# Kernel tuning notes

Hardware: AMD Instinct MI355X
Metric: run time of the kernel (lower is better)

Reference implementation:

```python
import jax, jax.numpy as jnp
import numpy as np

N, E = 50000, 800000
DIN, DH, H, DOUT = 128, 16, 8, 32  # hidden = H*DH = 128
NEG_SLOPE = 0.2


def setup_inputs() -> dict:
    key = jax.random.key(0)
    ks = jax.random.split(key, 10)
    g = lambda k, shape, fan: jax.random.normal(k, shape, jnp.float32) * (1.0 / np.sqrt(fan))
    return {
        "x": jax.random.normal(ks[0], (N, DIN), jnp.float32),
        "edge_index": jax.random.randint(ks[1], (2, E), 0, N, dtype=jnp.int64),
        # layer 1 (GATv2Conv(DIN, DH, heads=H), concat=True)
        "W1_src": g(ks[2], (DIN, H * DH), DIN),
        "W1_dst": g(ks[3], (DIN, H * DH), DIN),
        "b1_src": jnp.zeros((H * DH,), jnp.float32),
        "b1_dst": jnp.zeros((H * DH,), jnp.float32),
        "att1": g(ks[4], (H, DH), DH),
        "bias1": jnp.zeros((H * DH,), jnp.float32),
        # layer 2 (GATv2Conv(H*DH, DOUT, heads=1))
        "W2_src": g(ks[5], (H * DH, DOUT), H * DH),
        "W2_dst": g(ks[6], (H * DH, DOUT), H * DH),
        "b2_src": jnp.zeros((DOUT,), jnp.float32),
        "b2_dst": jnp.zeros((DOUT,), jnp.float32),
        "att2": g(ks[7], (1, DOUT), DOUT),
        "bias2": jnp.zeros((DOUT,), jnp.float32),
    }


def _gatv2(x, src, dst, Wsrc, Wdst, bsrc, bdst, att, bias):
    # GATv2 conv: e_ij = att . LeakyReLU(Wsrc x_j + Wdst x_i); softmax over j->i; out_i = sum alpha_ij * Wsrc x_j
    n = x.shape[0]
    h, c = att.shape
    xs = (x @ Wsrc + bsrc).reshape(n, h, c)  # source transform (messages)
    xd = (x @ Wdst + bdst).reshape(n, h, c)  # target transform
    msg = xs[src]  # [Etot, h, c]
    e = jax.nn.leaky_relu(msg + xd[dst], NEG_SLOPE)
    logits = jnp.einsum('ehc,hc->eh', e, att)  # [Etot, h]
    m = jax.lax.stop_gradient(jax.ops.segment_max(logits, dst, num_segments=n))
    ex = jnp.exp(logits - m[dst])
    denom = jax.ops.segment_sum(ex, dst, num_segments=n)
    alpha = ex / denom[dst]  # edge softmax per target node, per head
    out = jax.ops.segment_sum(alpha[..., None] * msg, dst, num_segments=n)
    return out.reshape(n, h * c) + bias  # concat=True


def reference(x, edge_index, W1_src, W1_dst, b1_src, b1_dst, att1, bias1,
              W2_src, W2_dst, b2_src, b2_dst, att2, bias2):
    n = x.shape[0]
    loop = jnp.arange(n, dtype=edge_index.dtype)  # add_self_loops=True (PyG default)
    src = jnp.concatenate([edge_index[0], loop])
    dst = jnp.concatenate([edge_index[1], loop])
    h1 = _gatv2(x, src, dst, W1_src, W1_dst, b1_src, b1_dst, att1, bias1)
    h1 = jax.nn.elu(h1)
    h2 = _gatv2(h1, src, dst, W2_src, W2_dst, b2_src, b2_dst, att2, bias2)  # heads=1 -> [N, DOUT]
    return jax.nn.log_softmax(h2, axis=1)
```

## Files before the change

kernel.cpp:

```cpp
#include <hip/hip_runtime.h>
#include <math.h>

#define NEG_SLOPE 0.2f

typedef __attribute__((ext_vector_type(8))) _Float16 h8v;
typedef __attribute__((ext_vector_type(2))) _Float16 h2v;
typedef __attribute__((ext_vector_type(4))) float float4v;

__device__ __forceinline__ h2v u2h(unsigned u) { return __builtin_bit_cast(h2v, u); }
__device__ __forceinline__ unsigned h2u(h2v h) { return __builtin_bit_cast(unsigned, h); }
__device__ __forceinline__ unsigned pk16(float a, float b) {
  h2v r; r.x = (_Float16)a; r.y = (_Float16)b;
  return __builtin_bit_cast(unsigned, r);
}
__device__ __forceinline__ unsigned short f16b(float f) {
  return __builtin_bit_cast(unsigned short, (_Float16)f);
}
__device__ __forceinline__ float fdot2(h2v a, h2v b, float c) {
#if __has_builtin(__builtin_amdgcn_fdot2)
  return __builtin_amdgcn_fdot2(a, b, c, false);
#else
  return fmaf((float)a.x, (float)b.x, fmaf((float)a.y, (float)b.y, c));
#endif
}

__device__ __forceinline__ int block_scan256(int v, int tid, int* ws) {
  const int lane = tid & 63, w = tid >> 6;
  int incl = v;
#pragma unroll
  for (int off = 1; off < 64; off <<= 1) {
    int t = __shfl_up(incl, off);
    if (lane >= off) incl += t;
  }
  if (lane == 63) ws[w] = incl;
  __syncthreads();
  if (tid == 0) {
    int s = 0;
#pragma unroll
    for (int i = 0; i < 4; i++) { int t = ws[i]; ws[4 + i] = s; s += t; }
  }
  __syncthreads();
  return incl - v + ws[4 + w];
}

__global__ __launch_bounds__(256) void pack_hist(
    const float* __restrict__ W1s, const float* __restrict__ W1d,
    const float* __restrict__ W2s, const float* __restrict__ W2d,
    unsigned short* __restrict__ B1s, unsigned short* __restrict__ B1d,
    unsigned short* __restrict__ B2s, unsigned short* __restrict__ B2d,
    const int* __restrict__ ei, int* __restrict__ bhist, int N, int E, int NB) {
  int blk = blockIdx.x;
  if (blk < 20) {
    const float* W; unsigned short* Bp; int C, base;
    if (blk < 8)       { W = W1s; Bp = B1s; C = 128; base = blk; }
    else if (blk < 16) { W = W1d; Bp = B1d; C = 128; base = blk - 8; }
    else if (blk < 18) { W = W2s; Bp = B2s; C = 32;  base = blk - 16; }
    else               { W = W2d; Bp = B2d; C = 32;  base = blk - 18; }
    int idx = base * 256 + threadIdx.x;
    int total = (C / 16) * 4 * 64;
    if (idx >= total) return;
    int lane = idx & 63;
    int kc = (idx >> 6) & 3;
    int t = idx >> 8;
    int n = t * 16 + (lane & 15);
    int k0 = kc * 32 + (lane >> 4) * 8;
    unsigned short* o = Bp + (size_t)idx * 8;
#pragma unroll
    for (int j = 0; j < 8; j++) o[j] = f16b(W[(size_t)(k0 + j) * C + n]);
    return;
  }
  blk -= 20;
  __shared__ int cnt[256];
  const int tid = threadIdx.x;
  cnt[tid] = 0;
  __syncthreads();
  const int base = blk * 4096;
  const int vn = min(4096, E - base);
#pragma unroll 4
  for (int j = 0; j < 16; j++) {
    int i = j * 256 + tid;
    if (i < vn) {
      int d = ei[E + base + i];
      d = min(max(d, 0), N - 1);
      atomicAdd(&cnt[d >> 8], 1);
    }
  }
  __syncthreads();
  if (tid < NB && cnt[tid]) atomicAdd(&bhist[tid], cnt[tid]);
}

__global__ __launch_bounds__(256) void bucket_scan(
    const int* __restrict__ bhist, int* __restrict__ bbase,
    int* __restrict__ bcur, int NB) {
  __shared__ int ws[8];
  const int tid = threadIdx.x;
  int v = (tid < NB) ? bhist[tid] : 0;
  int excl = block_scan256(v, tid, ws);
  if (tid <= NB) bbase[tid] = excl;
  if (tid < NB) bcur[tid] = excl;
}

__global__ __launch_bounds__(256) void bucket_sort(
    const int* __restrict__ ei, int* __restrict__ bcur,
    unsigned int* __restrict__ pairs, int N, int E, int NB) {
  __shared__ int cnt[256];
  __shared__ int offs[256];
  __shared__ int gbase[256];
  __shared__ int lcur[256];
  __shared__ int ws[8];
  __shared__ unsigned int packed_s[4096];
  __shared__ unsigned char bucket_of[4096];
  const int tid = threadIdx.x;
  cnt[tid] = 0;
  __syncthreads();
  const int base = blockIdx.x * 4096;
  const int vn = min(4096, E - base);
#pragma unroll 4
  for (int j = 0; j < 16; j++) {
    int i = j * 256 + tid;
    if (i < vn) {
      int d = ei[E + base + i];
      d = min(max(d, 0), N - 1);
      atomicAdd(&cnt[d >> 8], 1);
    }
  }
  __syncthreads();
  int excl = block_scan256(cnt[tid], tid, ws);
  offs[tid] = excl;
  lcur[tid] = excl;
  if (tid < NB && cnt[tid]) gbase[tid] = atomicAdd(&bcur[tid], cnt[tid]);
  __syncthreads();
#pragma unroll 4
  for (int j = 0; j < 16; j++) {
    int i = j * 256 + tid;
    if (i < vn) {
      int s = ei[base + i];
      int d = ei[E + base + i];
      s = min(max(s, 0), N - 1);
      d = min(max(d, 0), N - 1);
      int b = d >> 8;
      int slot = atomicAdd(&lcur[b], 1);
      packed_s[slot] = (unsigned)s | ((unsigned)(d & 255) << 16);
      bucket_of[slot] = (unsigned char)b;
    }
  }
  __syncthreads();
  for (int i = tid; i < vn; i += 256) {
    int b = bucket_of[i];
    pairs[gbase[b] + (i - offs[b])] = packed_s[i];
  }
}

__global__ __launch_bounds__(256) void csr_fine(
    const unsigned int* __restrict__ pairs, const int* __restrict__ bbase,
    int* __restrict__ row_ofs, int* __restrict__ src_sorted, int N, int E, int NB) {
  __shared__ int cnt[256];
  __shared__ int cursor[256];
  __shared__ int ws[8];
  const int tid = threadIdx.x;
  const int b = blockIdx.x;
  const int d0 = b << 8;
  const int nd = min(256, N - d0);
  const int pbase = bbase[b];
  const int pcnt = bbase[b + 1] - pbase;
  const int row_base = pbase + d0;
  cnt[tid] = (tid < nd) ? 1 : 0;
  __syncthreads();
  for (int i = tid; i < pcnt; i += 256) {
    unsigned p = pairs[pbase + i];
    atomicAdd(&cnt[(p >> 16) & 255], 1);
  }
  __syncthreads();
  int excl = block_scan256(cnt[tid], tid, ws);
  if (tid < nd) {
    row_ofs[d0 + tid] = row_base + excl;
    src_sorted[row_base + excl] = d0 + tid;
    cursor[tid] = excl + 1;
  }
  if (b == NB - 1 && tid == 0) row_ofs[N] = E + N;
  __syncthreads();
  for (int i = tid; i < pcnt; i += 256) {
    unsigned p = pairs[pbase + i];
    int dl = (p >> 16) & 255;
    int slot = atomicAdd(&cursor[dl], 1);
    src_sorted[row_base + slot] = (int)(p & 0xffffu);
  }
}

template <int NT, int CVT>
__global__ __launch_bounds__(256) void mfma_xform2(
    const void* __restrict__ Xin,
    const unsigned short* __restrict__ BpS, const unsigned short* __restrict__ BpD,
    const float* __restrict__ bS, const float* __restrict__ bD,
    unsigned int* __restrict__ Ys, unsigned int* __restrict__ Yd, int M) {
  const int wave = threadIdx.x >> 6;
  const int lane = threadIdx.x & 63;
  const int row0 = blockIdx.x * 64 + wave * 16;
  const int m = lane & 15, q = lane >> 4;
  const int arow = min(row0 + m, M - 1);
  h8v a[4];
  if constexpr (CVT) {
    const float* xp = (const float*)Xin + (size_t)arow * 128 + q * 8;
#pragma unroll
    for (int kc = 0; kc < 4; kc++) {
      const float4 f0 = *(const float4*)(xp + kc * 32);
      const float4 f1 = *(const float4*)(xp + kc * 32 + 4);
      uint4 u;
      u.x = pk16(f0.x, f0.y); u.y = pk16(f0.z, f0.w);
      u.z = pk16(f1.x, f1.y); u.w = pk16(f1.z, f1.w);
      a[kc] = __builtin_bit_cast(h8v, u);
    }
  } else {
    const unsigned short* xp = (const unsigned short*)Xin + (size_t)arow * 128 + q * 8;
#pragma unroll
    for (int kc = 0; kc < 4; kc++) a[kc] = *(const h8v*)(xp + kc * 32);
  }
  float4v accS[NT], accD[NT];
#pragma unroll
  for (int t = 0; t < NT; t++) { accS[t] = (float4v)(0.f); accD[t] = (float4v)(0.f); }
#pragma unroll
  for (int kc = 0; kc < 4; kc++) {
#pragma unroll
    for (int t = 0; t < NT; t++) {
      h8v bs = *(const h8v*)(BpS + ((size_t)(t * 4 + kc) * 64 + lane) * 8);
      h8v bd = *(const h8v*)(BpD + ((size_t)(t * 4 + kc) * 64 + lane) * 8);
      accS[t] = __builtin_amdgcn_mfma_f32_16x16x32_f16(a[kc], bs, accS[t], 0, 0, 0);
      accD[t] = __builtin_amdgcn_mfma_f32_16x16x32_f16(a[kc], bd, accD[t], 0, 0, 0);
    }
  }
  const bool even = (m & 1) == 0;
#pragma unroll
  for (int t = 0; t < NT; t++) {
    const int col = t * 16 + m;
    const float bcS = bS[col], bcD = bD[col];
#pragma unroll
    for (int r = 0; r < 4; r++) {
      const int row = row0 + q * 4 + r;
      float vS = accS[t][r] + bcS;
      float vD = accD[t][r] + bcD;
      float pS = __shfl_xor(vS, 1);
      float pD = __shfl_xor(vD, 1);
      if (even && row < M) {
        size_t idx = (size_t)row * (NT * 8) + t * 8 + (m >> 1);
        Ys[idx] = pk16(vS, pS);
        Yd[idx] = pk16(vD, pD);
      }
    }
  }
}

__global__ __launch_bounds__(256) void gat1_fused(
    const int* __restrict__ row_ofs, const int* __restrict__ src_sorted,
    const unsigned int* __restrict__ xsb, const unsigned int* __restrict__ xdb,
    const float* __restrict__ att, const float* __restrict__ bias,
    unsigned int* __restrict__ h1b, int N) {
  const int node = (int)((blockIdx.x * 256u + threadIdx.x) >> 6);
  const int lane = threadIdx.x & 63;
  const int l = lane & 15;
  const int g = lane >> 4;
  if (node >= N) return;
  h2v at2[4], xd[4];
  {
    const float4 a01 = *(const float4*)(att + 8 * l);
    const float4 a23 = *(const float4*)(att + 8 * l + 4);
    at2[0] = u2h(pk16(a01.x, a01.y)); at2[1] = u2h(pk16(a01.z, a01.w));
    at2[2] = u2h(pk16(a23.x, a23.y)); at2[3] = u2h(pk16(a23.z, a23.w));
    const uint4 xdp = *(const uint4*)(xdb + (unsigned)(node * 64 + 4 * l));
    xd[0] = u2h(xdp.x); xd[1] = u2h(xdp.y);
    xd[2] = u2h(xdp.z); xd[3] = u2h(xdp.w);
  }
  h2v ns; ns.x = (_Float16)NEG_SLOPE; ns.y = (_Float16)NEG_SLOPE;
  h2v acc[4];
#pragma unroll
  for (int i = 0; i < 4; i++) acc[i] = (h2v)((_Float16)0.f);
  float den = 0.f;
  const int b = row_ofs[node];
  const int cnt = row_ofs[node + 1] - b;
  for (int base = 0; base < cnt; base += 64) {
    const int rem = cnt - base;
    int sidx = (lane < rem) ? src_sorted[b + base + lane] : node;
    const int nIter = min(16, (rem + 3) >> 2);
    int s = __shfl(sidx, g);
    uint4 mp = *(const uint4*)(xsb + (unsigned)(s * 64 + 4 * l));
    for (int it = 0; it < nIter; it++) {
      const uint4 cur = mp;
      const bool v = (base + 4 * it + g) < cnt;
      if (it + 1 < nIter) {
        int sn = __shfl(sidx, 4 * (it + 1) + g);
        mp = *(const uint4*)(xsb + (unsigned)(sn * 64 + 4 * l));
      }
      const h2v m0 = u2h(cur.x), m1 = u2h(cur.y), m2 = u2h(cur.z), m3 = u2h(cur.w);
      h2v t0 = m0 + xd[0]; h2v r0 = __builtin_elementwise_max(t0, t0 * ns);
      h2v t1 = m1 + xd[1]; h2v r1 = __builtin_elementwise_max(t1, t1 * ns);
      h2v t2 = m2 + xd[2]; h2v r2 = __builtin_elementwise_max(t2, t2 * ns);
      h2v t3 = m3 + xd[3]; h2v r3 = __builtin_elementwise_max(t3, t3 * ns);
      float p = fdot2(r0, at2[0], 0.f);
      p = fdot2(r1, at2[1], p);
      p = fdot2(r2, at2[2], p);
      p = fdot2(r3, at2[3], p);
      p += __shfl_xor(p, 1);
      float ex = v ? __expf(p) : 0.f;
      den += ex;
      h2v exh; exh.x = exh.y = (_Float16)ex;
      acc[0] += m0 * exh;
      acc[1] += m1 * exh;
      acc[2] += m2 * exh;
      acc[3] += m3 * exh;
    }
  }
#pragma unroll
  for (int off = 16; off < 64; off <<= 1) {
#pragma unroll
    for (int i = 0; i < 4; i++) acc[i] += u2h(__shfl_xor(h2u(acc[i]), off));
    den += __shfl_xor(den, off);
  }
  if (lane < 16) {
    const float inv = 1.f / den;
    const float4 bc01 = *(const float4*)(bias + 8 * l);
    const float4 bc23 = *(const float4*)(bias + 8 * l + 4);
    float v0 = fmaf((float)acc[0].x, inv, bc01.x);
    float v1 = fmaf((float)acc[0].y, inv, bc01.y);
    float v2 = fmaf((float)acc[1].x, inv, bc01.z);
    float v3 = fmaf((float)acc[1].y, inv, bc01.w);
    float v4 = fmaf((float)acc[2].x, inv, bc23.x);
    float v5 = fmaf((float)acc[2].y, inv, bc23.y);
    float v6 = fmaf((float)acc[3].x, inv, bc23.z);
    float v7 = fmaf((float)acc[3].y, inv, bc23.w);
    v0 = v0 > 0.f ? v0 : __expf(v0) - 1.f;
    v1 = v1 > 0.f ? v1 : __expf(v1) - 1.f;
    v2 = v2 > 0.f ? v2 : __expf(v2) - 1.f;
    v3 = v3 > 0.f ? v3 : __expf(v3) - 1.f;
    v4 = v4 > 0.f ? v4 : __expf(v4) - 1.f;
    v5 = v5 > 0.f ? v5 : __expf(v5) - 1.f;
    v6 = v6 > 0.f ? v6 : __expf(v6) - 1.f;
    v7 = v7 > 0.f ? v7 : __expf(v7) - 1.f;
    uint4 o;
    o.x = pk16(v0, v1); o.y = pk16(v2, v3);
    o.z = pk16(v4, v5); o.w = pk16(v6, v7);
    *(uint4*)(h1b + (unsigned)(node * 64 + 4 * l)) = o;
  }
}

__global__ __launch_bounds__(256) void gat2_fused(
    const int* __restrict__ row_ofs, const int* __restrict__ src_sorted,
    const unsigned int* __restrict__ xsb, const unsigned int* __restrict__ xdb,
    const float* __restrict__ att, const float* __restrict__ bias,
    float* __restrict__ out, int N) {
  const int node = (int)((blockIdx.x * 256u + threadIdx.x) >> 6);
  const int lane = threadIdx.x & 63;
  const int l = lane & 3;
  const int g = lane >> 2;
  if (node >= N) return;
  h2v at2[4], xd[4];
  {
    const float4 a01 = *(const float4*)(att + 8 * l);
    const float4 a23 = *(const float4*)(att + 8 * l + 4);
    at2[0] = u2h(pk16(a01.x, a01.y)); at2[1] = u2h(pk16(a01.z, a01.w));
    at2[2] = u2h(pk16(a23.x, a23.y)); at2[3] = u2h(pk16(a23.z, a23.w));
    const uint4 xdp = *(const uint4*)(xdb + (unsigned)(node * 16 + 4 * l));
    xd[0] = u2h(xdp.x); xd[1] = u2h(xdp.y);
    xd[2] = u2h(xdp.z); xd[3] = u2h(xdp.w);
  }
  h2v ns; ns.x = (_Float16)NEG_SLOPE; ns.y = (_Float16)NEG_SLOPE;
  h2v acc[4];
#pragma unroll
  for (int i = 0; i < 4; i++) acc[i] = (h2v)((_Float16)0.f);
  float den = 0.f;
  const int b = row_ofs[node];
  const int cnt = row_ofs[node + 1] - b;
  for (int base = 0; base < cnt; base += 64) {
    const int rem = cnt - base;
    int sidx = (lane < rem) ? src_sorted[b + base + lane] : node;
    const int nIter = min(4, (rem + 15) >> 4);
    int s = __shfl(sidx, g);
    uint4 mp = *(const uint4*)(xsb + (unsigned)(s * 16 + 4 * l));
    for (int it = 0; it < nIter; it++) {
      const uint4 cur = mp;
      const bool v = (base + 16 * it + g) < cnt;
      if (it + 1 < nIter) {
        int sn = __shfl(sidx, 16 * (it + 1) + g);
        mp = *(const uint4*)(xsb + (unsigned)(sn * 16 + 4 * l));
      }
      const h2v m0 = u2h(cur.x), m1 = u2h(cur.y), m2 = u2h(cur.z), m3 = u2h(cur.w);
      h2v t0 = m0 + xd[0]; h2v r0 = __builtin_elementwise_max(t0, t0 * ns);
      h2v t1 = m1 + xd[1]; h2v r1 = __builtin_elementwise_max(t1, t1 * ns);
      h2v t2 = m2 + xd[2]; h2v r2 = __builtin_elementwise_max(t2, t2 * ns);
      h2v t3 = m3 + xd[3]; h2v r3 = __builtin_elementwise_max(t3, t3 * ns);
      float p = fdot2(r0, at2[0], 0.f);
      p = fdot2(r1, at2[1], p);
      p = fdot2(r2, at2[2], p);
      p = fdot2(r3, at2[3], p);
      p += __shfl_xor(p, 1);
      p += __shfl_xor(p, 2);
      float ex = v ? __expf(p) : 0.f;
      den += ex;
      h2v exh; exh.x = exh.y = (_Float16)ex;
      acc[0] += m0 * exh;
      acc[1] += m1 * exh;
      acc[2] += m2 * exh;
      acc[3] += m3 * exh;
    }
  }
#pragma unroll
  for (int off = 4; off < 64; off <<= 1) {
#pragma unroll
    for (int i = 0; i < 4; i++) acc[i] += u2h(__shfl_xor(h2u(acc[i]), off));
    den += __shfl_xor(den, off);
  }
  if (lane < 4) {
    const float inv = 1.f / den;
    const float4 bc01 = *(const float4*)(bias + 8 * l);
    const float4 bc23 = *(const float4*)(bias + 8 * l + 4);
    float v0 = fmaf((float)acc[0].x, inv, bc01.x);
    float v1 = fmaf((float)acc[0].y, inv, bc01.y);
    float v2 = fmaf((float)acc[1].x, inv, bc01.z);
    float v3 = fmaf((float)acc[1].y, inv, bc01.w);
    float v4 = fmaf((float)acc[2].x, inv, bc23.x);
    float v5 = fmaf((float)acc[2].y, inv, bc23.y);
    float v6 = fmaf((float)acc[3].x, inv, bc23.z);
    float v7 = fmaf((float)acc[3].y, inv, bc23.w);
    float mx = fmaxf(fmaxf(fmaxf(v0, v1), fmaxf(v2, v3)),
                     fmaxf(fmaxf(v4, v5), fmaxf(v6, v7)));
    mx = fmaxf(mx, __shfl_xor(mx, 1));
    mx = fmaxf(mx, __shfl_xor(mx, 2));
    float sum = __expf(v0 - mx) + __expf(v1 - mx) + __expf(v2 - mx) +
                __expf(v3 - mx) + __expf(v4 - mx) + __expf(v5 - mx) +
                __expf(v6 - mx) + __expf(v7 - mx);
    sum += __shfl_xor(sum, 1);
    sum += __shfl_xor(sum, 2);
    const float lse = mx + __logf(sum);
    float* op = out + (size_t)node * 32 + 8 * l;
    *(float4*)op = make_float4(v0 - lse, v1 - lse, v2 - lse, v3 - lse);
    *(float4*)(op + 4) = make_float4(v4 - lse, v5 - lse, v6 - lse, v7 - lse);
  }
}

extern "C" void kernel_launch(void* const* d_in, const int* in_sizes, int n_in,
                              void* d_out, int out_size, void* d_ws, size_t ws_size,
                              hipStream_t stream) {
  const float* x = (const float*)d_in[0];
  const int* ei = (const int*)d_in[1];
  const float* W1s = (const float*)d_in[2];
  const float* W1d = (const float*)d_in[3];
  const float* b1s = (const float*)d_in[4];
  const float* b1d = (const float*)d_in[5];
  const float* att1 = (const float*)d_in[6];
  const float* bias1 = (const float*)d_in[7];
  const float* W2s = (const float*)d_in[8];
  const float* W2d = (const float*)d_in[9];
  const float* b2s = (const float*)d_in[10];
  const float* b2d = (const float*)d_in[11];
  const float* att2 = (const float*)d_in[12];
  const float* bias2 = (const float*)d_in[13];
  float* out = (float*)d_out;

  const int N = in_sizes[0] / 128;
  const int E = in_sizes[1] / 2;
  const int NB = (N + 255) >> 8;

  char* p = (char*)d_ws;
  auto alloc = [&](size_t bytes) { char* r = p; p += (bytes + 63) & ~63ull; return r; };
  unsigned int* xs1b = (unsigned int*)alloc((size_t)N * 64 * 4);
  unsigned int* xd1b = (unsigned int*)alloc((size_t)N * 64 * 4);
  unsigned int* xs2b = (unsigned int*)alloc((size_t)N * 16 * 4);
  unsigned int* xd2b = (unsigned int*)alloc((size_t)N * 16 * 4);
  unsigned int* h1b = (unsigned int*)alloc((size_t)N * 64 * 4);
  unsigned short* Bp1s = (unsigned short*)alloc(8 * 4 * 64 * 8 * 2);
  unsigned short* Bp1d = (unsigned short*)alloc(8 * 4 * 64 * 8 * 2);
  unsigned short* Bp2s = (unsigned short*)alloc(2 * 4 * 64 * 8 * 2);
  unsigned short* Bp2d = (unsigned short*)alloc(2 * 4 * 64 * 8 * 2);
  int* bhist = (int*)alloc((size_t)NB * 4);
  int* bbase = (int*)alloc((size_t)(NB + 1) * 4);
  int* bcur = (int*)alloc((size_t)NB * 4);
  unsigned int* pairs = (unsigned int*)alloc((size_t)E * 4);
  int* row_ofs = (int*)alloc((size_t)(N + 1) * 4);
  int* src_sorted = (int*)alloc((size_t)(E + N) * 4);

  hipMemsetAsync(bhist, 0, (size_t)NB * sizeof(int), stream);

  const int nA = (E + 4095) / 4096;
  pack_hist<<<20 + nA, 256, 0, stream>>>(W1s, W1d, W2s, W2d, Bp1s, Bp1d, Bp2s, Bp2d,
                                         ei, bhist, N, E, NB);
  bucket_scan<<<1, 256, 0, stream>>>(bhist, bbase, bcur, NB);
  bucket_sort<<<nA, 256, 0, stream>>>(ei, bcur, pairs, N, E, NB);
  csr_fine<<<NB, 256, 0, stream>>>(pairs, bbase, row_ofs, src_sorted, N, E, NB);

  const int xblocks = (N + 63) / 64;
  mfma_xform2<8, 1><<<xblocks, 256, 0, stream>>>(x, Bp1s, Bp1d, b1s, b1d, xs1b, xd1b, N);

  gat1_fused<<<(N + 3) / 4, 256, 0, stream>>>(row_ofs, src_sorted, xs1b, xd1b,
                                              att1, bias1, h1b, N);

  mfma_xform2<2, 0><<<xblocks, 256, 0, stream>>>(h1b, Bp2s, Bp2d, b2s, b2d,
                                                 xs2b, xd2b, N);

  gat2_fused<<<(N + 3) / 4, 256, 0, stream>>>(row_ofs, src_sorted, xs2b, xd2b,
                                              att2, bias2, out, N);
}
```

Baseline: 220.3 us.

## Fold bucket scan into sort/CSR kernels and widen gat1 lanes per edge

After: 222.7 us. No clear change (+1.1%).

```diff
diff --git a/kernel.cpp b/kernel.cpp
--- a/kernel.cpp
+++ b/kernel.cpp
@@ -89,19 +89,9 @@
   if (tid < NB && cnt[tid]) atomicAdd(&bhist[tid], cnt[tid]);
 }
 
-__global__ __launch_bounds__(256) void bucket_scan(
-    const int* __restrict__ bhist, int* __restrict__ bbase,
-    int* __restrict__ bcur, int NB) {
-  __shared__ int ws[8];
-  const int tid = threadIdx.x;
-  int v = (tid < NB) ? bhist[tid] : 0;
-  int excl = block_scan256(v, tid, ws);
-  if (tid <= NB) bbase[tid] = excl;
-  if (tid < NB) bcur[tid] = excl;
-}
-
 __global__ __launch_bounds__(256) void bucket_sort(
-    const int* __restrict__ ei, int* __restrict__ bcur,
+    const int* __restrict__ ei, const int* __restrict__ bhist,
+    int* __restrict__ bcur_rel,
     unsigned int* __restrict__ pairs, int N, int E, int NB) {
   __shared__ int cnt[256];
   __shared__ int offs[256];
@@ -128,7 +118,8 @@
   int excl = block_scan256(cnt[tid], tid, ws);
   offs[tid] = excl;
   lcur[tid] = excl;
-  if (tid < NB && cnt[tid]) gbase[tid] = atomicAdd(&bcur[tid], cnt[tid]);
+  int bb = block_scan256((tid < NB) ? bhist[tid] : 0, tid, ws);
+  if (tid < NB && cnt[tid]) gbase[tid] = bb + atomicAdd(&bcur_rel[tid], cnt[tid]);
   __syncthreads();
 #pragma unroll 4
   for (int j = 0; j < 16; j++) {
@@ -152,20 +143,24 @@
 }
 
 __global__ __launch_bounds__(256) void csr_fine(
-    const unsigned int* __restrict__ pairs, const int* __restrict__ bbase,
+    const unsigned int* __restrict__ pairs, const int* __restrict__ bhist,
     int* __restrict__ row_ofs, int* __restrict__ src_sorted, int N, int E, int NB) {
   __shared__ int cnt[256];
   __shared__ int cursor[256];
   __shared__ int ws[8];
+  __shared__ int pb[2];
   const int tid = threadIdx.x;
   const int b = blockIdx.x;
   const int d0 = b << 8;
   const int nd = min(256, N - d0);
-  const int pbase = bbase[b];
-  const int pcnt = bbase[b + 1] - pbase;
+  cnt[tid] = (tid < nd) ? 1 : 0;
+  int bb = block_scan256((tid < NB) ? bhist[tid] : 0, tid, ws);
+  if (tid == b) pb[0] = bb;
+  if (tid == b + 1) pb[1] = bb;
+  __syncthreads();
+  const int pbase = pb[0];
+  const int pcnt = pb[1] - pbase;
   const int row_base = pbase + d0;
-  cnt[tid] = (tid < nd) ? 1 : 0;
-  __syncthreads();
   for (int i = tid; i < pcnt; i += 256) {
     unsigned p = pairs[pbase + i];
     atomicAdd(&cnt[(p >> 16) & 255], 1);
@@ -256,88 +251,101 @@
     unsigned int* __restrict__ h1b, int N) {
   const int node = (int)((blockIdx.x * 256u + threadIdx.x) >> 6);
   const int lane = threadIdx.x & 63;
-  const int l = lane & 15;
-  const int g = lane >> 4;
+  const int j = lane & 7;
+  const int g = lane >> 3;
   if (node >= N) return;
-  h2v at2[4], xd[4];
+  h2v at2[8], xd[8];
   {
-    const float4 a01 = *(const float4*)(att + 8 * l);
-    const float4 a23 = *(const float4*)(att + 8 * l + 4);
-    at2[0] = u2h(pk16(a01.x, a01.y)); at2[1] = u2h(pk16(a01.z, a01.w));
-    at2[2] = u2h(pk16(a23.x, a23.y)); at2[3] = u2h(pk16(a23.z, a23.w));
-    const uint4 xdp = *(const uint4*)(xdb + (unsigned)(node * 64 + 4 * l));
-    xd[0] = u2h(xdp.x); xd[1] = u2h(xdp.y);
-    xd[2] = u2h(xdp.z); xd[3] = u2h(xdp.w);
+    const float4 a0 = *(const float4*)(att + 16 * j);
+    const float4 a1 = *(const float4*)(att + 16 * j + 4);
+    const float4 a2 = *(const float4*)(att + 16 * j + 8);
+    const float4 a3 = *(const float4*)(att + 16 * j + 12);
+    at2[0] = u2h(pk16(a0.x, a0.y)); at2[1] = u2h(pk16(a0.z, a0.w));
+    at2[2] = u2h(pk16(a1.x, a1.y)); at2[3] = u2h(pk16(a1.z, a1.w));
+    at2[4] = u2h(pk16(a2.x, a2.y)); at2[5] = u2h(pk16(a2.z, a2.w));
+    at2[6] = u2h(pk16(a3.x, a3.y)); at2[7] = u2h(pk16(a3.z, a3.w));
+    const uint4 x0 = *(const uint4*)(xdb + (unsigned)(node * 64 + 8 * j));
+    const uint4 x1 = *(const uint4*)(xdb + (unsigned)(node * 64 + 8 * j + 4));
+    xd[0] = u2h(x0.x); xd[1] = u2h(x0.y); xd[2] = u2h(x0.z); xd[3] = u2h(x0.w);
+    xd[4] = u2h(x1.x); xd[5] = u2h(x1.y); xd[6] = u2h(x1.z); xd[7] = u2h(x1.w);
   }
   h2v ns; ns.x = (_Float16)NEG_SLOPE; ns.y = (_Float16)NEG_SLOPE;
-  h2v acc[4];
-#pragma unroll
-  for (int i = 0; i < 4; i++) acc[i] = (h2v)((_Float16)0.f);
+  h2v acc[8];
+#pragma unroll
+  for (int i = 0; i < 8; i++) acc[i] = (h2v)((_Float16)0.f);
   float den = 0.f;
   const int b = row_ofs[node];
   const int cnt = row_ofs[node + 1] - b;
   for (int base = 0; base < cnt; base += 64) {
     const int rem = cnt - base;
     int sidx = (lane < rem) ? src_sorted[b + base + lane] : node;
-    const int nIter = min(16, (rem + 3) >> 2);
+    const int nIter = min(8, (rem + 7) >> 3);
     int s = __shfl(sidx, g);
-    uint4 mp = *(const uint4*)(xsb + (unsigned)(s * 64 + 4 * l));
+    uint4 mA = *(const uint4*)(xsb + (unsigned)(s * 64 + 8 * j));
+    uint4 mB = *(const uint4*)(xsb + (unsigned)(s * 64 + 8 * j + 4));
     for (int it = 0; it < nIter; it++) {
-      const uint4 cur = mp;
-      const bool v = (base + 4 * it + g) < cnt;
+      const uint4 c0 = mA, c1 = mB;
+      const bool v = (base + 8 * it + g) < cnt;
       if (it + 1 < nIter) {
-        int sn = __shfl(sidx, 4 * (it + 1) + g);
-        mp = *(const uint4*)(xsb + (unsigned)(sn * 64 + 4 * l));
+        int sn = __shfl(sidx, 8 * (it + 1) + g);
+        mA = *(const uint4*)(xsb + (unsigned)(sn * 64 + 8 * j));
+        mB = *(const uint4*)(xsb + (unsigned)(sn * 64 + 8 * j + 4));
       }
-      const h2v m0 = u2h(cur.x), m1 = u2h(cur.y), m2 = u2h(cur.z), m3 = u2h(cur.w);
-      h2v t0 = m0 + xd[0]; h2v r0 = __builtin_elementwise_max(t0, t0 * ns);
-      h2v t1 = m1 + xd[1]; h2v r1 = __builtin_elementwise_max(t1, t1 * ns);
-      h2v t2 = m2 + xd[2]; h2v r2 = __builtin_elementwise_max(t2, t2 * ns);
-      h2v t3 = m3 + xd[3]; h2v r3 = __builtin_elementwise_max(t3, t3 * ns);
-      float p = fdot2(r0, at2[0], 0.f);
-      p = fdot2(r1, at2[1], p);
-      p = fdot2(r2, at2[2], p);
-      p = fdot2(r3, at2[3], p);
-      p += __shfl_xor(p, 1);
+      h2v m[8];
+      m[0] = u2h(c0.x); m[1] = u2h(c0.y); m[2] = u2h(c0.z); m[3] = u2h(c0.w);
+      m[4] = u2h(c1.x); m[5] = u2h(c1.y); m[6] = u2h(c1.z); m[7] = u2h(c1.w);
+      float p = 0.f;
+#pragma unroll
+      for (int k = 0; k < 8; k++) {
+        h2v t = m[k] + xd[k];
+        h2v r = __builtin_elementwise_max(t, t * ns);
+        p = fdot2(r, at2[k], p);
+      }
       float ex = v ? __expf(p) : 0.f;
       den += ex;
       h2v exh; exh.x = exh.y = (_Float16)ex;
-      acc[0] += m0 * exh;
-      acc[1] += m1 * exh;
-      acc[2] += m2 * exh;
-      acc[3] += m3 * exh;
-    }
-  }
-#pragma unroll
-  for (int off = 16; off < 64; off <<= 1) {
-#pragma unroll
-    for (int i = 0; i < 4; i++) acc[i] += u2h(__shfl_xor(h2u(acc[i]), off));
+#pragma unroll
+      for (int k = 0; k < 8; k++) acc[k] += m[k] * exh;
+    }
+  }
+#pragma unroll
+  for (int off = 8; off < 64; off <<= 1) {
+#pragma unroll
+    for (int i = 0; i < 8; i++) acc[i] += u2h(__shfl_xor(h2u(acc[i]), off));
     den += __shfl_xor(den, off);
   }
-  if (lane < 16) {
+  if (lane < 8) {
     const float inv = 1.f / den;
-    const float4 bc01 = *(const float4*)(bias + 8 * l);
-    const float4 bc23 = *(const float4*)(bias + 8 * l + 4);
-    float v0 = fmaf((float)acc[0].x, inv, bc01.x);
-    float v1 = fmaf((float)acc[0].y, inv, bc01.y);
-    float v2 = fmaf((float)acc[1].x, inv, bc01.z);
-    float v3 = fmaf((float)acc[1].y, inv, bc01.w);
-    float v4 = fmaf((float)acc[2].x, inv, bc23.x);
-    float v5 = fmaf((float)acc[2].y, inv, bc23.y);
-    float v6 = fmaf((float)acc[3].x, inv, bc23.z);
-    float v7 = fmaf((float)acc[3].y, inv, bc23.w);
-    v0 = v0 > 0.f ? v0 : __expf(v0) - 1.f;
-    v1 = v1 > 0.f ? v1 : __expf(v1) - 1.f;
-    v2 = v2 > 0.f ? v2 : __expf(v2) - 1.f;
-    v3 = v3 > 0.f ? v3 : __expf(v3) - 1.f;
-    v4 = v4 > 0.f ? v4 : __expf(v4) - 1.f;
-    v5 = v5 > 0.f ? v5 : __expf(v5) - 1.f;
-    v6 = v6 > 0.f ? v6 : __expf(v6) - 1.f;
-    v7 = v7 > 0.f ? v7 : __expf(v7) - 1.f;
-    uint4 o;
-    o.x = pk16(v0, v1); o.y = pk16(v2, v3);
-    o.z = pk16(v4, v5); o.w = pk16(v6, v7);
-    *(uint4*)(h1b + (unsigned)(node * 64 + 4 * l)) = o;
+    const float4 bc0 = *(const float4*)(bias + 16 * j);
+    const float4 bc1 = *(const float4*)(bias + 16 * j + 4);
+    const float4 bc2 = *(const float4*)(bias + 16 * j + 8);
+    const float4 bc3 = *(const float4*)(bias + 16 * j + 12);
+    float v[16];
+    v[0]  = fmaf((float)acc[0].x, inv, bc0.x);
+    v[1]  = fmaf((float)acc[0].y, inv, bc0.y);
+    v[2]  = fmaf((float)acc[1].x, inv, bc0.z);
+    v[3]  = fmaf((float)acc[1].y, inv, bc0.w);
+    v[4]  = fmaf((float)acc[2].x, inv, bc1.x);
+    v[5]  = fmaf((float)acc[2].y, inv, bc1.y);
+    v[6]  = fmaf((float)acc[3].x, inv, bc1.z);
+    v[7]  = fmaf((float)acc[3].y, inv, bc1.w);
+    v[8]  = fmaf((float)acc[4].x, inv, bc2.x);
+    v[9]  = fmaf((float)acc[4].y, inv, bc2.y);
+    v[10] = fmaf((float)acc[5].x, inv, bc2.z);
+    v[11] = fmaf((float)acc[5].y, inv, bc2.w);
+    v[12] = fmaf((float)acc[6].x, inv, bc3.x);
+    v[13] = fmaf((float)acc[6].y, inv, bc3.y);
+    v[14] = fmaf((float)acc[7].x, inv, bc3.z);
+    v[15] = fmaf((float)acc[7].y, inv, bc3.w);
+#pragma unroll
+    for (int k = 0; k < 16; k++) v[k] = v[k] > 0.f ? v[k] : __expf(v[k]) - 1.f;
+    uint4 o0, o1;
+    o0.x = pk16(v[0], v[1]);   o0.y = pk16(v[2], v[3]);
+    o0.z = pk16(v[4], v[5]);   o0.w = pk16(v[6], v[7]);
+    o1.x = pk16(v[8], v[9]);   o1.y = pk16(v[10], v[11]);
+    o1.z = pk16(v[12], v[13]); o1.w = pk16(v[14], v[15]);
+    *(uint4*)(h1b + (unsigned)(node * 64 + 8 * j)) = o0;
+    *(uint4*)(h1b + (unsigned)(node * 64 + 8 * j + 4)) = o1;
   }
 }
 
@@ -469,21 +477,19 @@
   unsigned short* Bp1d = (unsigned short*)alloc(8 * 4 * 64 * 8 * 2);
   unsigned short* Bp2s = (unsigned short*)alloc(2 * 4 * 64 * 8 * 2);
   unsigned short* Bp2d = (unsigned short*)alloc(2 * 4 * 64 * 8 * 2);
-  int* bhist = (int*)alloc((size_t)NB * 4);
-  int* bbase = (int*)alloc((size_t)(NB + 1) * 4);
-  int* bcur = (int*)alloc((size_t)NB * 4);
+  int* bhist = (int*)alloc(512 * 4);
+  int* bcur_rel = bhist + 256;
   unsigned int* pairs = (unsigned int*)alloc((size_t)E * 4);
   int* row_ofs = (int*)alloc((size_t)(N + 1) * 4);
   int* src_sorted = (int*)alloc((size_t)(E + N) * 4);
 
-  hipMemsetAsync(bhist, 0, (size_t)NB * sizeof(int), stream);
+  hipMemsetAsync(bhist, 0, 512 * sizeof(int), stream);
 
   const int nA = (E + 4095) / 4096;
   pack_hist<<<20 + nA, 256, 0, stream>>>(W1s, W1d, W2s, W2d, Bp1s, Bp1d, Bp2s, Bp2d,
                                          ei, bhist, N, E, NB);
-  bucket_scan<<<1, 256, 0, stream>>>(bhist, bbase, bcur, NB);
-  bucket_sort<<<nA, 256, 0, stream>>>(ei, bcur, pairs, N, E, NB);
-  csr_fine<<<NB, 256, 0, stream>>>(pairs, bbase, row_ofs, src_sorted, N, E, NB);
+  bucket_sort<<<nA, 256, 0, stream>>>(ei, bhist, bcur_rel, pairs, N, E, NB);
+  csr_fine<<<NB, 256, 0, stream>>>(pairs, bhist, row_ofs, src_sorted, N, E, NB);
 
   const int xblocks = (N + 63) / 64;
   mfma_xform2<8, 1><<<xblocks, 256, 0, stream>>>(x, Bp1s, Bp1d, b1s, b1d, xs1b, xd1b, N);
```

## Fuse bucket scan into sort and merge sort with layer-1 transform launch

Applied to the files above, without the earlier changes.

New measurement: 202.9 us. 7.9% less time.

```diff
diff --git a/kernel.cpp b/kernel.cpp
--- a/kernel.cpp
+++ b/kernel.cpp
@@ -89,20 +89,10 @@
   if (tid < NB && cnt[tid]) atomicAdd(&bhist[tid], cnt[tid]);
 }
 
-__global__ __launch_bounds__(256) void bucket_scan(
-    const int* __restrict__ bhist, int* __restrict__ bbase,
-    int* __restrict__ bcur, int NB) {
-  __shared__ int ws[8];
-  const int tid = threadIdx.x;
-  int v = (tid < NB) ? bhist[tid] : 0;
-  int excl = block_scan256(v, tid, ws);
-  if (tid <= NB) bbase[tid] = excl;
-  if (tid < NB) bcur[tid] = excl;
-}
-
-__global__ __launch_bounds__(256) void bucket_sort(
-    const int* __restrict__ ei, int* __restrict__ bcur,
-    unsigned int* __restrict__ pairs, int N, int E, int NB) {
+__device__ __forceinline__ void bucket_sort_body(
+    int blk, const int* __restrict__ ei, const int* __restrict__ bhist,
+    int* __restrict__ bcur_rel, unsigned int* __restrict__ pairs,
+    int N, int E, int NB) {
   __shared__ int cnt[256];
   __shared__ int offs[256];
   __shared__ int gbase[256];
@@ -113,7 +103,7 @@
   const int tid = threadIdx.x;
   cnt[tid] = 0;
   __syncthreads();
-  const int base = blockIdx.x * 4096;
+  const int base = blk * 4096;
   const int vn = min(4096, E - base);
 #pragma unroll 4
   for (int j = 0; j < 16; j++) {
@@ -128,7 +118,8 @@
   int excl = block_scan256(cnt[tid], tid, ws);
   offs[tid] = excl;
   lcur[tid] = excl;
-  if (tid < NB && cnt[tid]) gbase[tid] = atomicAdd(&bcur[tid], cnt[tid]);
+  int bb = block_scan256((tid < NB) ? bhist[tid] : 0, tid, ws);
+  if (tid < NB && cnt[tid]) gbase[tid] = bb + atomicAdd(&bcur_rel[tid], cnt[tid]);
   __syncthreads();
 #pragma unroll 4
   for (int j = 0; j < 16; j++) {
@@ -151,51 +142,15 @@
   }
 }
 
-__global__ __launch_bounds__(256) void csr_fine(
-    const unsigned int* __restrict__ pairs, const int* __restrict__ bbase,
-    int* __restrict__ row_ofs, int* __restrict__ src_sorted, int N, int E, int NB) {
-  __shared__ int cnt[256];
-  __shared__ int cursor[256];
-  __shared__ int ws[8];
-  const int tid = threadIdx.x;
-  const int b = blockIdx.x;
-  const int d0 = b << 8;
-  const int nd = min(256, N - d0);
-  const int pbase = bbase[b];
-  const int pcnt = bbase[b + 1] - pbase;
-  const int row_base = pbase + d0;
-  cnt[tid] = (tid < nd) ? 1 : 0;
-  __syncthreads();
-  for (int i = tid; i < pcnt; i += 256) {
-    unsigned p = pairs[pbase + i];
-    atomicAdd(&cnt[(p >> 16) & 255], 1);
-  }
-  __syncthreads();
-  int excl = block_scan256(cnt[tid], tid, ws);
-  if (tid < nd) {
-    row_ofs[d0 + tid] = row_base + excl;
-    src_sorted[row_base + excl] = d0 + tid;
-    cursor[tid] = excl + 1;
-  }
-  if (b == NB - 1 && tid == 0) row_ofs[N] = E + N;
-  __syncthreads();
-  for (int i = tid; i < pcnt; i += 256) {
-    unsigned p = pairs[pbase + i];
-    int dl = (p >> 16) & 255;
-    int slot = atomicAdd(&cursor[dl], 1);
-    src_sorted[row_base + slot] = (int)(p & 0xffffu);
-  }
-}
-
 template <int NT, int CVT>
-__global__ __launch_bounds__(256) void mfma_xform2(
-    const void* __restrict__ Xin,
+__device__ __forceinline__ void xform_body(
+    int blk, const void* __restrict__ Xin,
     const unsigned short* __restrict__ BpS, const unsigned short* __restrict__ BpD,
     const float* __restrict__ bS, const float* __restrict__ bD,
     unsigned int* __restrict__ Ys, unsigned int* __restrict__ Yd, int M) {
   const int wave = threadIdx.x >> 6;
   const int lane = threadIdx.x & 63;
-  const int row0 = blockIdx.x * 64 + wave * 16;
+  const int row0 = blk * 64 + wave * 16;
   const int m = lane & 15, q = lane >> 4;
   const int arow = min(row0 + m, M - 1);
   h8v a[4];
@@ -246,6 +201,69 @@
         Yd[idx] = pk16(vD, pD);
       }
     }
+  }
+}
+
+__global__ __launch_bounds__(256) void sort_xform(
+    const int* __restrict__ ei, const int* __restrict__ bhist,
+    int* __restrict__ bcur_rel, unsigned int* __restrict__ pairs,
+    const float* __restrict__ x,
+    const unsigned short* __restrict__ Bp1s, const unsigned short* __restrict__ Bp1d,
+    const float* __restrict__ b1s, const float* __restrict__ b1d,
+    unsigned int* __restrict__ xs1b, unsigned int* __restrict__ xd1b,
+    int N, int E, int NB, int nA) {
+  if ((int)blockIdx.x < nA) {
+    bucket_sort_body(blockIdx.x, ei, bhist, bcur_rel, pairs, N, E, NB);
+    return;
+  }
+  xform_body<8, 1>(blockIdx.x - nA, x, Bp1s, Bp1d, b1s, b1d, xs1b, xd1b, N);
+}
+
+__global__ __launch_bounds__(256) void mfma_xform_l2(
+    const void* __restrict__ Xin,
+    const unsigned short* __restrict__ BpS, const unsigned short* __restrict__ BpD,
+    const float* __restrict__ bS, const float* __restrict__ bD,
+    unsigned int* __restrict__ Ys, unsigned int* __restrict__ Yd, int M) {
+  xform_body<2, 0>(blockIdx.x, Xin, BpS, BpD, bS, bD, Ys, Yd, M);
+}
+
+__global__ __launch_bounds__(256) void csr_fine(
+    const unsigned int* __restrict__ pairs, const int* __restrict__ bhist,
+    int* __restrict__ row_ofs, int* __restrict__ src_sorted, int N, int E, int NB) {
+  __shared__ int cnt[256];
+  __shared__ int cursor[256];
+  __shared__ int ws[8];
+  __shared__ int pb[2];
+  const int tid = threadIdx.x;
+  const int b = blockIdx.x;
+  const int d0 = b << 8;
+  const int nd = min(256, N - d0);
+  cnt[tid] = (tid < nd) ? 1 : 0;
+  int bb = block_scan256((tid < NB) ? bhist[tid] : 0, tid, ws);
+  if (tid == b) pb[0] = bb;
+  if (tid == b + 1) pb[1] = bb;
+  __syncthreads();
+  const int pbase = pb[0];
+  const int pcnt = pb[1] - pbase;
+  const int row_base = pbase + d0;
+  for (int i = tid; i < pcnt; i += 256) {
+    unsigned p = pairs[pbase + i];
+    atomicAdd(&cnt[(p >> 16) & 255], 1);
+  }
+  __syncthreads();
+  int excl = block_scan256(cnt[tid], tid, ws);
+  if (tid < nd) {
+    row_ofs[d0 + tid] = row_base + excl;
+    src_sorted[row_base + excl] = d0 + tid;
+    cursor[tid] = excl + 1;
+  }
+  if (b == NB - 1 && tid == 0) row_ofs[N] = E + N;
+  __syncthreads();
+  for (int i = tid; i < pcnt; i += 256) {
+    unsigned p = pairs[pbase + i];
+    int dl = (p >> 16) & 255;
+    int slot = atomicAdd(&cursor[dl], 1);
+    src_sorted[row_base + slot] = (int)(p & 0xffffu);
   }
 }
 
@@ -469,30 +487,31 @@
   unsigned short* Bp1d = (unsigned short*)alloc(8 * 4 * 64 * 8 * 2);
   unsigned short* Bp2s = (unsigned short*)alloc(2 * 4 * 64 * 8 * 2);
   unsigned short* Bp2d = (unsigned short*)alloc(2 * 4 * 64 * 8 * 2);
-  int* bhist = (int*)alloc((size_t)NB * 4);
-  int* bbase = (int*)alloc((size_t)(NB + 1) * 4);
-  int* bcur = (int*)alloc((size_t)NB * 4);
+  int* bhist = (int*)alloc(512 * 4);
+  int* bcur_rel = bhist + 256;
   unsigned int* pairs = (unsigned int*)alloc((size_t)E * 4);
   int* row_ofs = (int*)alloc((size_t)(N + 1) * 4);
   int* src_sorted = (int*)alloc((size_t)(E + N) * 4);
 
-  hipMemsetAsync(bhist, 0, (size_t)NB * sizeof(int), stream);
+  hipMemsetAsync(bhist, 0, 512 * sizeof(int), stream);
 
   const int nA = (E + 4095) / 4096;
+  const int xblocks = (N + 63) / 64;
+
   pack_hist<<<20 + nA, 256, 0, stream>>>(W1s, W1d, W2s, W2d, Bp1s, Bp1d, Bp2s, Bp2d,
                                          ei, bhist, N, E, NB);
-  bucket_scan<<<1, 256, 0, stream>>>(bhist, bbase, bcur, NB);
-  bucket_sort<<<nA, 256, 0, stream>>>(ei, bcur, pairs, N, E, NB);
-  csr_fine<<<NB, 256, 0, stream>>>(pairs, bbase, row_ofs, src_sorted, N, E, NB);
-
-  const int xblocks = (N + 63) / 64;
-  mfma_xform2<8, 1><<<xblocks, 256, 0, stream>>>(x, Bp1s, Bp1d, b1s, b1d, xs1b, xd1b, N);
+
+  sort_xform<<<nA + xblocks, 256, 0, stream>>>(ei, bhist, bcur_rel, pairs,
+                                               x, Bp1s, Bp1d, b1s, b1d,
+                                               xs1b, xd1b, N, E, NB, nA);
+
+  csr_fine<<<NB, 256, 0, stream>>>(pairs, bhist, row_ofs, src_sorted, N, E, NB);
 
   gat1_fused<<<(N + 3) / 4, 256, 0, stream>>>(row_ofs, src_sorted, xs1b, xd1b,
                                               att1, bias1, h1b, N);
 
-  mfma_xform2<2, 0><<<xblocks, 256, 0, stream>>>(h1b, Bp2s, Bp2d, b2s, b2d,
-                                                 xs2b, xd2b, N);
+  mfma_xform_l2<<<xblocks, 256, 0, stream>>>(h1b, Bp2s, Bp2d, b2s, b2d,
+                                             xs2b, xd2b, N);
 
   gat2_fused<<<(N + 3) / 4, 256, 0, stream>>>(row_ofs, src_sorted, xs2b, xd2b,
                                               att2, bias2, out, N);
```
